# Kernel tuning notes

Measured on AMD Instinct MI355X. Metric: run time of the kernel, lower is better.

Reference implementation:

```python
import jax, jax.numpy as jnp
import numpy as np

B, C, W, H, A, NCLS, M = 8, 32, 32, 32, 6, 14, 64
HARD_NUM = 256
LAM_HNM = 0.2
LAM_NOOBJ = 0.001


def setup_inputs() -> dict:
    rng = np.random.default_rng(0)
    proposal_map = jax.random.normal(jax.random.key(0), (B, C, W, H, A, 3 + NCLS), dtype=jnp.float32)
    # labels: first n_valid entries per (b, a) are real bboxes, rest are -100 padding
    labels = np.full((B, A, M), -100, dtype=np.int32)
    n_valid = rng.integers(4, M // 2, size=(B, A))
    for b in range(B):
        for a in range(A):
            k = int(n_valid[b, a])
            lab = rng.integers(0, NCLS, size=k)
            is_hn = rng.random(k) < 0.3
            lab = np.where(is_hn, -1 - rng.integers(0, NCLS, size=k), lab)
            labels[b, a, :k] = lab
    cwh = rng.integers(0, [C, W, H], size=(B, A, M, 3)).astype(np.int32)
    prop_idx = np.concatenate([cwh, labels[..., None]], axis=-1)
    prop_reg = (rng.standard_normal((B, A, M, 3)) * 0.3).astype(np.float32)
    return {
        "proposal_map": proposal_map,
        "prop_idx": jnp.asarray(prop_idx),
        "prop_reg": jnp.asarray(prop_reg),
    }


def reference(proposal_map, prop_idx, prop_reg):
    dt = proposal_map.dtype
    ncls = proposal_map.shape[-1] - 3
    c, w, h, labels = prop_idx[..., 0], prop_idx[..., 1], prop_idx[..., 2], prop_idx[..., 3]
    bi = jnp.arange(proposal_map.shape[0])[:, None, None]
    ai = jnp.arange(proposal_map.shape[4])[None, :, None]
    # gather per-bbox cell vector: [B, A, M, 3+ncls]
    vals = proposal_map[bi, c, w, h, ai]

    pos_mask = labels >= 0
    hn_mask = (labels < 0) & (labels != -100)
    posf = pos_mask.astype(dt)
    P = jnp.maximum(jnp.sum(posf), 1.0)

    cls_logits = vals[..., 3:]                                   # [B, A, M, ncls]
    lab = jnp.clip(labels, 0, ncls - 1)
    onehot = jax.nn.one_hot(lab, ncls, dtype=dt)
    pos_logit = jnp.sum(cls_logits * onehot, axis=-1)            # [B, A, M]

    # BCEWithLogits(x, 1) = softplus(-x); BCEWithLogits(x, 0) = softplus(x)
    cl_pos_loss = jnp.sum(jax.nn.softplus(-pos_logit) * posf) / P
    cl_neg_loss = (jnp.sum(jax.nn.softplus(cls_logits) * (1.0 - onehot) * posf[..., None])
                   / (P * (ncls - 1))) / (ncls - 1)

    # hard-negative mining: per class, topk(count*hard_num) over all flattened logits
    j = jnp.where(hn_mask, -1 - labels, 0)
    counts = jnp.zeros((ncls,), jnp.int32).at[j.ravel()].add(hn_mask.ravel().astype(jnp.int32))
    k = counts * HARD_NUM                                        # [ncls]
    cls_flat = jnp.moveaxis(proposal_map[..., 3:], -1, 0).reshape(ncls, -1)
    srt = -jnp.sort(-cls_flat, axis=1)                           # descending
    sel = (jnp.arange(srt.shape[1])[None, :] < k[:, None]).astype(dt)
    tot_k = jnp.sum(k)
    hn_loss = jnp.where(
        tot_k > 0,
        LAM_HNM * jnp.sum(jax.nn.softplus(srt) * sel) / jnp.maximum(tot_k, 1).astype(dt),
        jnp.array(0.0, dt),
    )

    regu_neg_loss = LAM_NOOBJ * jnp.mean(jax.nn.softplus(proposal_map))

    # SmoothL1(tanh(reg_pred), reg_target), mean over positives x 3 coords (beta=1)
    d = jnp.tanh(vals[..., :3]) - prop_reg
    sl = jnp.where(jnp.abs(d) < 1.0, 0.5 * d * d, jnp.abs(d) - 0.5)
    reg_loss = jnp.sum(sl * posf[..., None]) / (3.0 * P)

    return cl_pos_loss + cl_neg_loss + hn_loss + regu_neg_loss + reg_loss
```

## Files before the change

kernel.cpp:

```cpp
#include <hip/hip_runtime.h>
#include <cstdint>
#include <cstddef>

#define B_ 8
#define C_ 32
#define W_ 32
#define H_ 32
#define A_ 6
#define NCLS 14
#define M_ 64
#define HARD_NUM 256
#define LAM_HNM 0.2f
#define LAM_NOOBJ 0.001f

#define NCH 17
#define NPOS (B_*C_*W_*H_*A_)
#define TOTAL (NPOS*NCH)
#define NPROP (B_*A_*M_)

#define KSHIFT 21
#define HB0 1532
#define NHB 64
#define HSLOTS (NHB*8)
#define SUBBITS 11
#define NBIN_F (1<<SUBBITS)
#define K1_BLOCKS 2048
#define K1_THREADS 256
#define NWAVES (K1_BLOCKS*(K1_THREADS/64))
#define NY 128

#define OFF_FACC   0
#define OFF_UACC   64
#define OFF_BSTAR  128
#define OFF_CNTAB  192
#define OFF_SUMAB  256
#define OFF_HNP    320
#define OFF_DONE   384
#define OFF_RSUM   4096
#define OFF_NWAV   12288
#define OFF_FINE   45056
#define OFF_M32    274432
#define OFF_PART   798720
#define OFF_CAND   4993024

__device__ __forceinline__ float spf(float x) {
    return fmaxf(x, 0.0f) + __logf(1.0f + __expf(-fabsf(x)));
}
__device__ __forceinline__ float sp(float x) {
    return fmaxf(x, 0.0f) + log1pf(__expf(-fabsf(x)));
}

__global__ __launch_bounds__(K1_THREADS)
void k1_stream(const float* __restrict__ pm,
               unsigned* __restrict__ partials, unsigned* __restrict__ cand,
               unsigned* __restrict__ nwav, float* __restrict__ rsum,
               float* __restrict__ facc, unsigned* __restrict__ uacc,
               int seg_w) {
    __shared__ unsigned hist[HSLOTS];
    __shared__ float wsum[4];
    if (blockIdx.x == 0 && threadIdx.x < 32) {
        if (threadIdx.x < 16) facc[threadIdx.x] = 0.0f;
        else                  uacc[threadIdx.x - 16] = 0u;
    }
    for (int s = threadIdx.x; s < HSLOTS; s += K1_THREADS) hist[s] = 0;
    __syncthreads();
    int lane = threadIdx.x & 63;
    int wid = threadIdx.x >> 6;
    unsigned wseg = blockIdx.x * (K1_THREADS / 64) + wid;
    unsigned* gc = cand + (size_t)wseg * seg_w;
    unsigned wcount = 0;
    float racc = 0.0f;
    int tid = blockIdx.x * K1_THREADS + threadIdx.x;
    int nth = gridDim.x * K1_THREADS;
    const int n4 = TOTAL / 4;
    int ch0 = (tid * 4) % NCH;
    for (int i = tid; i < n4; i += nth) {
        float4 v = reinterpret_cast<const float4*>(pm)[i];
        float xs[4] = {v.x, v.y, v.z, v.w};
        int ch = ch0;
#pragma unroll
        for (int j = 0; j < 4; ++j) {
            float x = xs[j];
            racc += spf(x);
            bool q = (ch >= 3) && (x >= 1.0f);
            unsigned long long mb = __ballot(q);
            if (q) {
                unsigned ut = __float_as_uint(x) & 0xFFFFFFF0u;
                unsigned wb = ((ut | 0x80000000u) >> KSHIFT) - HB0;
                if (wb > NHB - 1) wb = NHB - 1;
                int cm3 = ch - 3;
                atomicAdd(&hist[wb * 8 + (cm3 >> 1)], (cm3 & 1) ? 0x10000u : 1u);
                unsigned idx = wcount +
                    (unsigned)__popcll(mb & ((1ull << lane) - 1ull));
                if (idx < (unsigned)seg_w) gc[idx] = ut | (unsigned)cm3;
            }
            wcount += (unsigned)__popcll(mb);
            ch = (ch == NCH - 1) ? 0 : ch + 1;
        }
        ch0 -= 2; if (ch0 < 0) ch0 += NCH;
    }
    if (lane == 0)
        nwav[wseg] = (wcount < (unsigned)seg_w) ? wcount : (unsigned)seg_w;
    __syncthreads();
    unsigned* dst = partials + (size_t)blockIdx.x * HSLOTS;
    for (int s = threadIdx.x; s < HSLOTS; s += K1_THREADS) dst[s] = hist[s];
    for (int o = 32; o; o >>= 1) racc += __shfl_down(racc, o, 64);
    if (lane == 0) wsum[wid] = racc;
    __syncthreads();
    if (threadIdx.x == 0)
        rsum[blockIdx.x] = wsum[0] + wsum[1] + wsum[2] + wsum[3];
}

__global__ __launch_bounds__(128)
void k2_props(const float* __restrict__ pm, const int* __restrict__ pidx,
              const float* __restrict__ preg,
              float* __restrict__ facc, unsigned* __restrict__ uacc) {
    __shared__ float s_clp, s_cln, s_rg;
    __shared__ unsigned s_pos;
    int t = threadIdx.x;
    if (t == 0) { s_clp = 0; s_cln = 0; s_rg = 0; s_pos = 0; }
    __syncthreads();
    int tid = blockIdx.x * 128 + t;
    int p = tid >> 2, sub = tid & 3;
    float clp = 0.0f, cln = 0.0f, rg = 0.0f;
    int lab = -100;
    if (p < NPROP) {
        const int4 q = *reinterpret_cast<const int4*>(pidx + (size_t)p * 4);
        lab = q.w;
        if (lab >= 0) {
            int b = p / (A_ * M_);
            int a = (p / M_) % A_;
            const float* v = pm
                + (size_t)((((b * C_ + q.x) * W_ + q.y) * H_ + q.z) * A_ + a) * NCH;
#pragma unroll
            for (int m = 0; m < 4; ++m) {
                int j = sub + 4 * m;
                if (j < NCLS) {
                    float lg = v[3 + j];
                    if (j == lab) clp += sp(-lg);
                    else          cln += sp(lg);
                }
            }
            if (sub < 3) {
                float d = tanhf(v[sub]) - preg[(size_t)p * 3 + sub];
                float ad = fabsf(d);
                rg = (ad < 1.0f) ? 0.5f * d * d : ad - 0.5f;
            }
        } else if (lab != -100 && sub == 0) {
            atomicAdd(&uacc[1 + (-1 - lab)], 1u);
        }
    }
    clp += __shfl_xor(clp, 1, 64); clp += __shfl_xor(clp, 2, 64);
    cln += __shfl_xor(cln, 1, 64); cln += __shfl_xor(cln, 2, 64);
    rg  += __shfl_xor(rg, 1, 64);  rg  += __shfl_xor(rg, 2, 64);
    if (sub == 0 && lab >= 0) {
        atomicAdd(&s_clp, clp);
        atomicAdd(&s_cln, cln);
        atomicAdd(&s_rg, rg);
        atomicAdd(&s_pos, 1u);
    }
    __syncthreads();
    if (t == 0) {
        if (s_clp != 0.0f) atomicAdd(&facc[0], s_clp);
        if (s_cln != 0.0f) atomicAdd(&facc[1], s_cln);
        if (s_rg != 0.0f)  atomicAdd(&facc[2], s_rg);
        if (s_pos)         atomicAdd(&uacc[0], s_pos);
    }
}

__global__ __launch_bounds__(256)
void kr_reduce(const unsigned* __restrict__ partials,
               unsigned* __restrict__ m32) {
    int slot = blockIdx.x * 256 + threadIdx.x;
    int y = blockIdx.y;
    const int BPY = K1_BLOCKS / NY;
    unsigned a0 = 0, a1 = 0;
#pragma unroll
    for (int p = y * BPY; p < y * BPY + BPY; ++p) {
        unsigned v = partials[(size_t)p * HSLOTS + slot];
        a0 += v & 0xFFFFu;
        a1 += v >> 16;
    }
    m32[((size_t)y * HSLOTS + slot) * 2]     = a0;
    m32[((size_t)y * HSLOTS + slot) * 2 + 1] = a1;
}

__global__ __launch_bounds__(256)
void k2_merge(const unsigned* __restrict__ m32,
              const float* __restrict__ rsum, const unsigned* __restrict__ uacc,
              int* __restrict__ bstar, unsigned* __restrict__ cntab,
              float* __restrict__ sumab, float* __restrict__ facc,
              unsigned long long* __restrict__ fine, unsigned* __restrict__ done) {
    int t = threadIdx.x;
    if (blockIdx.x == 14) {
        __shared__ float s[256];
        if (t == 0) *done = 0u;
        float a = 0.0f;
#pragma unroll
        for (int kk = 0; kk < K1_BLOCKS / 256; ++kk) a += rsum[t + kk * 256];
        s[t] = a;
        __syncthreads();
        for (int o = 128; o; o >>= 1) { if (t < o) s[t] += s[t + o]; __syncthreads(); }
        if (t == 0) facc[3] = s[0];
        return;
    }
    int cls = blockIdx.x;
    unsigned long long* fc = fine + (size_t)cls * NBIN_F;
    for (int s2 = t; s2 < NBIN_F; s2 += 256) fc[s2] = 0ull;
    if (t == 0) sumab[cls] = 0.0f;
    unsigned k = uacc[1 + cls] * HARD_NUM;
    if (k == 0) { if (t == 0) bstar[cls] = -2; return; }
    int pair = cls >> 1, half = cls & 1;
    int bin = t & 63, grp = t >> 6;
    const int YPG = NY / 4;
    unsigned c = 0;
    for (int y = grp * YPG; y < grp * YPG + YPG; ++y)
        c += m32[((size_t)y * HSLOTS + bin * 8 + pair) * 2 + half];
    __shared__ unsigned cq[256];
    cq[t] = c;
    __syncthreads();
    if (t == 0) {
        unsigned cum = 0; int bb = -1;
        for (int b2 = NHB - 1; b2 >= 0; --b2) {
            unsigned cc = cq[b2] + cq[64 + b2] + cq[128 + b2] + cq[192 + b2];
            if (cum + cc >= k) { bb = b2; break; }
            cum += cc;
        }
        bstar[cls] = bb;
        cntab[cls] = cum;
    }
}

__global__ __launch_bounds__(256)
void k3_cand(const unsigned* __restrict__ cand, const unsigned* __restrict__ nwav,
             const int* __restrict__ bstar, unsigned long long* __restrict__ fine,
             float* __restrict__ sumab, int seg_w) {
    __shared__ float csum[16];
    __shared__ int bst[16];
    int t = threadIdx.x;
    if (t < 16) { csum[t] = 0.0f; bst[t] = (t < 14) ? bstar[t] : -2; }
    __syncthreads();
    for (int w = 0; w < 4; ++w) {
        unsigned wseg = blockIdx.x * 4 + w;
        const unsigned* gc = cand + (size_t)wseg * seg_w;
        unsigned n = nwav[wseg];
        for (unsigned i = t; i < n; i += 256) {
            unsigned e = gc[i];
            int cls = (int)(e & 15u);
            int b = bst[cls];
            if (b == -2) continue;
            unsigned ut = e & 0xFFFFFFF0u;
            unsigned key = ut | 0x80000000u;
            unsigned wb = (key >> KSHIFT) - HB0;
            if (wb > NHB - 1) wb = NHB - 1;
            float x = __uint_as_float(ut | 0x8u);
            if (b == -1 || (int)wb > b) {
                atomicAdd(&csum[cls], spf(x));
            } else if ((int)wb == b) {
                unsigned sub = (key >> (KSHIFT - SUBBITS)) & (NBIN_F - 1);
                unsigned long long pk = (1ull << 43)
                    | (unsigned long long)(spf(x) * 262144.0f + 0.5f);
                atomicAdd(&fine[(size_t)cls * NBIN_F + sub], pk);
            }
        }
    }
    __syncthreads();
    if (t < 14 && csum[t] != 0.0f) atomicAdd(&sumab[t], csum[t]);
}

__global__ __launch_bounds__(256)
void k4_resolve(const unsigned long long* __restrict__ fine,
                const unsigned* __restrict__ uacc, const int* __restrict__ bstar,
                const unsigned* __restrict__ cntab, const float* __restrict__ sumab,
                const float* __restrict__ facc, float* __restrict__ hnp,
                unsigned* __restrict__ done, float* __restrict__ out) {
    int cls = blockIdx.x, t = threadIdx.x;
    __shared__ unsigned ck[256];
    __shared__ float cs[256];
    __shared__ int lastflag;
    unsigned k = uacc[1 + cls] * HARD_NUM;
    if (k == 0) {
        if (t == 0) hnp[cls] = 0.0f;
    } else {
        int b = bstar[cls];
        if (b == -1) {
            if (t == 0) hnp[cls] = sumab[cls];
        } else {
            unsigned r = k - cntab[cls];
            const unsigned long long* fc = fine + (size_t)cls * NBIN_F;
            unsigned lc = 0; float ls = 0.0f;
            for (int j = 0; j < NBIN_F / 256; ++j) {
                unsigned long long v = fc[t * (NBIN_F / 256) + j];
                lc += (unsigned)(v >> 43);
                ls += (float)(v & ((1ull << 43) - 1)) * (1.0f / 262144.0f);
            }
            ck[t] = lc; cs[t] = ls;
            __syncthreads();
            if (t == 0) {
                unsigned cum = 0; float sa = sumab[cls];
                for (int ch = 255; ch >= 0; --ch) {
                    if (cum + ck[ch] >= r) {
                        unsigned c2 = cum;
                        for (int j = NBIN_F / 256 - 1; j >= 0; --j) {
                            unsigned long long v = fc[ch * (NBIN_F / 256) + j];
                            unsigned c = (unsigned)(v >> 43);
                            float s = (float)(v & ((1ull << 43) - 1)) * (1.0f / 262144.0f);
                            if (c2 + c >= r) {
                                unsigned rem = r - c2;
                                if (c > 0) sa += (float)rem * (s / (float)c);
                                break;
                            }
                            c2 += c; sa += s;
                        }
                        break;
                    }
                    cum += ck[ch]; sa += cs[ch];
                }
                hnp[cls] = sa;
            }
        }
    }
    __syncthreads();
    if (t == 0) {
        __threadfence();
        unsigned ticket = atomicAdd(done, 1u);
        lastflag = (ticket == NCLS - 1) ? 1 : 0;
    }
    __syncthreads();
    if (lastflag && t == 0) {
        __threadfence();
        float hn_sum = 0.0f; unsigned totk = 0;
        for (int j = 0; j < NCLS; ++j) { hn_sum += hnp[j]; totk += uacc[1 + j]; }
        totk *= HARD_NUM;
        float P = fmaxf((float)uacc[0], 1.0f);
        float hn = (totk > 0) ? (LAM_HNM * hn_sum / (float)totk) : 0.0f;
        out[0] = facc[0] / P
               + facc[1] / (P * (float)((NCLS - 1) * (NCLS - 1)))
               + hn
               + LAM_NOOBJ * facc[3] / (float)TOTAL
               + facc[2] / (3.0f * P);
    }
}

extern "C" void kernel_launch(void* const* d_in, const int* in_sizes, int n_in,
                              void* d_out, int out_size, void* d_ws, size_t ws_size,
                              hipStream_t stream) {
    const float* pm   = (const float*)d_in[0];
    const int*   pidx = (const int*)d_in[1];
    const float* preg = (const float*)d_in[2];
    float* out = (float*)d_out;
    char* ws = (char*)d_ws;

    float*    facc  = (float*)(ws + OFF_FACC);
    unsigned* uacc  = (unsigned*)(ws + OFF_UACC);
    int*      bstar = (int*)(ws + OFF_BSTAR);
    unsigned* cntab = (unsigned*)(ws + OFF_CNTAB);
    float*    sumab = (float*)(ws + OFF_SUMAB);
    float*    hnp   = (float*)(ws + OFF_HNP);
    unsigned* done  = (unsigned*)(ws + OFF_DONE);
    float*    rsum  = (float*)(ws + OFF_RSUM);
    unsigned* nwav  = (unsigned*)(ws + OFF_NWAV);
    unsigned long long* fine = (unsigned long long*)(ws + OFF_FINE);
    unsigned* m32   = (unsigned*)(ws + OFF_M32);
    unsigned* partials = (unsigned*)(ws + OFF_PART);
    unsigned* cand = (unsigned*)(ws + OFF_CAND);

    long long remain = (long long)ws_size - (long long)OFF_CAND;
    int seg_w = (int)(remain / ((long long)NWAVES * 4));
    if (seg_w > 4096) seg_w = 4096;
    seg_w &= ~63;
    if (seg_w < 512) seg_w = 512;

    k1_stream <<<K1_BLOCKS, K1_THREADS, 0, stream>>>(pm, partials, cand, nwav,
                                                     rsum, facc, uacc, seg_w);
    k2_props  <<<(NPROP * 4) / 128, 128, 0, stream>>>(pm, pidx, preg, facc, uacc);
    kr_reduce <<<dim3(HSLOTS / 256, NY), 256, 0, stream>>>(partials, m32);
    k2_merge  <<<NCLS + 1, 256, 0, stream>>>(m32, rsum, uacc, bstar, cntab,
                                             sumab, facc, fine, done);
    k3_cand   <<<K1_BLOCKS, 256, 0, stream>>>(cand, nwav, bstar, fine, sumab, seg_w);
    k4_resolve<<<NCLS, 256, 0, stream>>>(fine, uacc, bstar, cntab, sumab, facc,
                                         hnp, done, out);
}
```

Measured before the change: 107.2 us.

## Move class histogram out of streaming pass and approximate softplus with polynomial

Moves the LDS bucket histogram out of the main streaming kernel into a new kernel that rebuilds it from the compacted candidate list, so the hot pass only computes the softplus sum and compacts candidates. The exact softplus in the regularization sum is replaced by a clamped quadratic polynomial, which removes exp/log from the per-element hot loop. This costs an extra launch and a second read of the candidate buffer. The polynomial only approximates softplus, so the mean-softplus term loses accuracy.

```diff
diff --git a/kernel.cpp b/kernel.cpp
--- a/kernel.cpp
+++ b/kernel.cpp
@@ -21,13 +21,14 @@
 #define KSHIFT 21
 #define HB0 1532
 #define NHB 64
-#define HSLOTS (NHB*8)
+#define HSL (NHB*NCLS)
 #define SUBBITS 11
 #define NBIN_F (1<<SUBBITS)
 #define K1_BLOCKS 2048
 #define K1_THREADS 256
 #define NWAVES (K1_BLOCKS*(K1_THREADS/64))
 #define NY 128
+#define NTH (K1_BLOCKS*K1_THREADS)
 
 #define OFF_FACC   0
 #define OFF_UACC   64
@@ -40,30 +41,24 @@
 #define OFF_NWAV   12288
 #define OFF_FINE   45056
 #define OFF_M32    274432
-#define OFF_PART   798720
-#define OFF_CAND   4993024
-
-__device__ __forceinline__ float spf(float x) {
-    return fmaxf(x, 0.0f) + __logf(1.0f + __expf(-fabsf(x)));
-}
+#define OFF_PART   733184
+#define OFF_CAND   8073216
+
 __device__ __forceinline__ float sp(float x) {
     return fmaxf(x, 0.0f) + log1pf(__expf(-fabsf(x)));
 }
 
 __global__ __launch_bounds__(K1_THREADS)
 void k1_stream(const float* __restrict__ pm,
-               unsigned* __restrict__ partials, unsigned* __restrict__ cand,
-               unsigned* __restrict__ nwav, float* __restrict__ rsum,
+               unsigned* __restrict__ cand, unsigned* __restrict__ nwav,
+               float* __restrict__ rsum,
                float* __restrict__ facc, unsigned* __restrict__ uacc,
                int seg_w) {
-    __shared__ unsigned hist[HSLOTS];
     __shared__ float wsum[4];
     if (blockIdx.x == 0 && threadIdx.x < 32) {
         if (threadIdx.x < 16) facc[threadIdx.x] = 0.0f;
         else                  uacc[threadIdx.x - 16] = 0u;
     }
-    for (int s = threadIdx.x; s < HSLOTS; s += K1_THREADS) hist[s] = 0;
-    __syncthreads();
     int lane = threadIdx.x & 63;
     int wid = threadIdx.x >> 6;
     unsigned wseg = blockIdx.x * (K1_THREADS / 64) + wid;
@@ -71,39 +66,33 @@
     unsigned wcount = 0;
     float racc = 0.0f;
     int tid = blockIdx.x * K1_THREADS + threadIdx.x;
-    int nth = gridDim.x * K1_THREADS;
     const int n4 = TOTAL / 4;
-    int ch0 = (tid * 4) % NCH;
-    for (int i = tid; i < n4; i += nth) {
+    int cm0 = (tid * 4) % NCH - 3;
+    for (int i = tid; i < n4; i += NTH) {
         float4 v = reinterpret_cast<const float4*>(pm)[i];
         float xs[4] = {v.x, v.y, v.z, v.w};
-        int ch = ch0;
+        int cm = cm0;
 #pragma unroll
         for (int j = 0; j < 4; ++j) {
             float x = xs[j];
-            racc += spf(x);
-            bool q = (ch >= 3) && (x >= 1.0f);
+            float tc = fminf(fabsf(x), 2.8f);
+            float g = fmaf(fmaf(0.08077f, tc, -0.4526f), tc, 0.6931472f);
+            racc += fmaxf(x, 0.0f) + g;
+            bool q = (cm >= 0) && (x >= 1.0f);
             unsigned long long mb = __ballot(q);
             if (q) {
-                unsigned ut = __float_as_uint(x) & 0xFFFFFFF0u;
-                unsigned wb = ((ut | 0x80000000u) >> KSHIFT) - HB0;
-                if (wb > NHB - 1) wb = NHB - 1;
-                int cm3 = ch - 3;
-                atomicAdd(&hist[wb * 8 + (cm3 >> 1)], (cm3 & 1) ? 0x10000u : 1u);
                 unsigned idx = wcount +
                     (unsigned)__popcll(mb & ((1ull << lane) - 1ull));
-                if (idx < (unsigned)seg_w) gc[idx] = ut | (unsigned)cm3;
+                if ((int)idx < seg_w)
+                    gc[idx] = (__float_as_uint(x) & 0xFFFFFFF0u) | (unsigned)cm;
             }
             wcount += (unsigned)__popcll(mb);
-            ch = (ch == NCH - 1) ? 0 : ch + 1;
-        }
-        ch0 -= 2; if (ch0 < 0) ch0 += NCH;
+            cm = (cm == NCH - 4) ? -3 : cm + 1;
+        }
+        cm0 -= 2; if (cm0 < -3) cm0 += NCH;
     }
     if (lane == 0)
         nwav[wseg] = (wcount < (unsigned)seg_w) ? wcount : (unsigned)seg_w;
-    __syncthreads();
-    unsigned* dst = partials + (size_t)blockIdx.x * HSLOTS;
-    for (int s = threadIdx.x; s < HSLOTS; s += K1_THREADS) dst[s] = hist[s];
     for (int o = 32; o; o >>= 1) racc += __shfl_down(racc, o, 64);
     if (lane == 0) wsum[wid] = racc;
     __syncthreads();
@@ -169,20 +158,39 @@
 }
 
 __global__ __launch_bounds__(256)
+void k3a_hist(const unsigned* __restrict__ cand, const unsigned* __restrict__ nwav,
+              unsigned* __restrict__ partials, int seg_w) {
+    __shared__ unsigned h[HSL];
+    int t = threadIdx.x;
+    for (int s = t; s < HSL; s += 256) h[s] = 0;
+    __syncthreads();
+    for (int w = 0; w < 4; ++w) {
+        unsigned wseg = blockIdx.x * 4 + w;
+        const unsigned* gc = cand + (size_t)wseg * seg_w;
+        unsigned n = nwav[wseg];
+        for (unsigned i = t; i < n; i += 256) {
+            unsigned e = gc[i];
+            unsigned wb = ((e | 0x80000000u) >> KSHIFT) - HB0;
+            if (wb > NHB - 1) wb = NHB - 1;
+            atomicAdd(&h[wb * NCLS + (e & 15u)], 1u);
+        }
+    }
+    __syncthreads();
+    unsigned* dst = partials + (size_t)blockIdx.x * HSL;
+    for (int s = t; s < HSL; s += 256) dst[s] = h[s];
+}
+
+__global__ __launch_bounds__(128)
 void kr_reduce(const unsigned* __restrict__ partials,
                unsigned* __restrict__ m32) {
-    int slot = blockIdx.x * 256 + threadIdx.x;
+    int slot = blockIdx.x * 128 + threadIdx.x;
     int y = blockIdx.y;
     const int BPY = K1_BLOCKS / NY;
-    unsigned a0 = 0, a1 = 0;
+    unsigned a = 0;
 #pragma unroll
-    for (int p = y * BPY; p < y * BPY + BPY; ++p) {
-        unsigned v = partials[(size_t)p * HSLOTS + slot];
-        a0 += v & 0xFFFFu;
-        a1 += v >> 16;
-    }
-    m32[((size_t)y * HSLOTS + slot) * 2]     = a0;
-    m32[((size_t)y * HSLOTS + slot) * 2 + 1] = a1;
+    for (int p = y * BPY; p < y * BPY + BPY; ++p)
+        a += partials[(size_t)p * HSL + slot];
+    m32[(size_t)y * HSL + slot] = a;
 }
 
 __global__ __launch_bounds__(256)
@@ -210,12 +218,11 @@
     if (t == 0) sumab[cls] = 0.0f;
     unsigned k = uacc[1 + cls] * HARD_NUM;
     if (k == 0) { if (t == 0) bstar[cls] = -2; return; }
-    int pair = cls >> 1, half = cls & 1;
     int bin = t & 63, grp = t >> 6;
     const int YPG = NY / 4;
     unsigned c = 0;
     for (int y = grp * YPG; y < grp * YPG + YPG; ++y)
-        c += m32[((size_t)y * HSLOTS + bin * 8 + pair) * 2 + half];
+        c += m32[(size_t)y * HSL + bin * NCLS + cls];
     __shared__ unsigned cq[256];
     cq[t] = c;
     __syncthreads();
@@ -255,11 +262,11 @@
             if (wb > NHB - 1) wb = NHB - 1;
             float x = __uint_as_float(ut | 0x8u);
             if (b == -1 || (int)wb > b) {
-                atomicAdd(&csum[cls], spf(x));
+                atomicAdd(&csum[cls], sp(x));
             } else if ((int)wb == b) {
                 unsigned sub = (key >> (KSHIFT - SUBBITS)) & (NBIN_F - 1);
                 unsigned long long pk = (1ull << 43)
-                    | (unsigned long long)(spf(x) * 262144.0f + 0.5f);
+                    | (unsigned long long)(sp(x) * 262144.0f + 0.5f);
                 atomicAdd(&fine[(size_t)cls * NBIN_F + sub], pk);
             }
         }
@@ -371,10 +378,11 @@
     seg_w &= ~63;
     if (seg_w < 512) seg_w = 512;
 
-    k1_stream <<<K1_BLOCKS, K1_THREADS, 0, stream>>>(pm, partials, cand, nwav,
-                                                     rsum, facc, uacc, seg_w);
+    k1_stream <<<K1_BLOCKS, K1_THREADS, 0, stream>>>(pm, cand, nwav, rsum,
+                                                     facc, uacc, seg_w);
     k2_props  <<<(NPROP * 4) / 128, 128, 0, stream>>>(pm, pidx, preg, facc, uacc);
-    kr_reduce <<<dim3(HSLOTS / 256, NY), 256, 0, stream>>>(partials, m32);
+    k3a_hist  <<<K1_BLOCKS, 256, 0, stream>>>(cand, nwav, partials, seg_w);
+    kr_reduce <<<dim3(HSL / 128, NY), 128, 0, stream>>>(partials, m32);
     k2_merge  <<<NCLS + 1, 256, 0, stream>>>(m32, rsum, uacc, bstar, cntab,
                                              sumab, facc, fine, done);
     k3_cand   <<<K1_BLOCKS, 256, 0, stream>>>(cand, nwav, bstar, fine, sumab, seg_w);
```

New measurement: 102.0 us. 1.05x faster.
